# Kernel tuning notes

Measured on AMD Instinct MI355X. Metric: run time of the kernel, lower is better.

The kernel has to match this reference:

```python
import jax, jax.numpy as jnp
import numpy as np

N, C, H, W = 1024, 16, 32, 32
E = 4096


def setup_inputs() -> dict:
    key = jax.random.key(0)
    ks = jax.random.split(key, 10)
    feats = jax.random.normal(ks[0], (N, C, H, W), dtype=jnp.float32)
    src = jax.random.randint(ks[1], (E,), 0, N)
    dst = jax.random.randint(ks[2], (E,), 0, N)
    sign = jax.random.randint(ks[3], (E,), 0, 2) * 2 - 1  # values in {-1, +1}
    edges = jnp.stack([src, sign, dst], axis=1).astype(jnp.int64)
    s = 0.05
    w1 = jax.random.normal(ks[4], (2 * C, 3 * C, 3, 3), dtype=jnp.float32) * s
    b1 = jnp.zeros((2 * C,), dtype=jnp.float32)
    w2 = jax.random.normal(ks[5], (2 * C, 2 * C, 3, 3), dtype=jnp.float32) * s
    b2 = jnp.zeros((2 * C,), dtype=jnp.float32)
    w3 = jax.random.normal(ks[6], (C, 2 * C, 3, 3), dtype=jnp.float32) * s
    b3 = jnp.zeros((C,), dtype=jnp.float32)
    return {"feats": feats, "edges": edges, "w1": w1, "b1": b1,
            "w2": w2, "b2": b2, "w3": w3, "b3": b3}


def _pool_edges(edges, feats, positive):
    # Bidirectional gather + scatter_add over selected edges.
    # Mask-by-zero keeps shapes static (equivalent math to torch.where selection).
    sign = edges[:, 1]
    mask = (sign > 0) if positive else (sign < 0)
    w = mask.astype(feats.dtype)[:, None, None, None]
    src = edges[:, 0]
    dst = edges[:, 2]
    pooled = jnp.zeros_like(feats)
    pooled = pooled.at[dst].add(feats[src] * w)  # src -> dst
    pooled = pooled.at[src].add(feats[dst] * w)  # dst -> src
    return pooled


def _conv(x, w, b):
    y = jax.lax.conv_general_dilated(
        x, w, window_strides=(1, 1), padding=((1, 1), (1, 1)),
        dimension_numbers=("NCHW", "OIHW", "NCHW"))
    return y + b[None, :, None, None]


def _leaky(x):
    return jax.nn.leaky_relu(x, negative_slope=0.1)


def reference(feats, edges, w1, b1, w2, b2, w3, b3):
    pos = _pool_edges(edges, feats, positive=True)
    neg = _pool_edges(edges, feats, positive=False)
    x = jnp.concatenate([feats, pos, neg], axis=1)  # [N, 3C, H, W]
    x = _leaky(_conv(x, w1, b1))
    x = _leaky(_conv(x, w2, b2))
    x = _leaky(_conv(x, w3, b3))
    return x
```

## Files before the change

### kernel.cpp

```cpp
#include <hip/hip_runtime.h>


#define NIMG 1024
#define CHW  16384
#define NEDGE 4096
#define MAXD 64

#define ICP1 56
#define ICP2 40
#define XSZ (34*34*ICP1)
#define WSZ (14*32*32)

#define WG1N (14*32*32)
#define WG2N (9*32*32)
#define WG3N (9*16*32)
#define WGTOT (WG1N+WG2N+WG3N)

typedef __attribute__((ext_vector_type(8))) _Float16 half8;
typedef __attribute__((ext_vector_type(4))) _Float16 half4;
typedef __attribute__((ext_vector_type(4))) float float4v;

__device__ __forceinline__ float leaky(float x) { return x > 0.f ? x : 0.1f * x; }

__global__ __launch_bounds__(256) void prep_kernel(
    const float* __restrict__ feats, _Float16* __restrict__ fcl,
    const int* __restrict__ edges, int* __restrict__ deg, int* __restrict__ adj,
    const float* __restrict__ w1, const float* __restrict__ w2,
    const float* __restrict__ w3, _Float16* __restrict__ wg)
{
    const int b = blockIdx.x, tid = threadIdx.x;
    if (b < NIMG) {
        const int n = b;
        const float* fb = feats + (size_t)n * CHW;
        _Float16*    ob = fcl   + (size_t)n * 1024 * 16;
        const int p0 = tid * 4;
        float4v t[16];
        #pragma unroll
        for (int c = 0; c < 16; ++c) t[c] = *(const float4v*)(fb + (c << 10) + p0);
        #pragma unroll
        for (int u = 0; u < 4; ++u) {
            half8 v0, v1;
            #pragma unroll
            for (int c = 0; c < 8; ++c) { v0[c] = (_Float16)t[c][u]; v1[c] = (_Float16)t[c+8][u]; }
            *(half8*)(ob + (p0+u)*16)     = v0;
            *(half8*)(ob + (p0+u)*16 + 8) = v1;
        }
        return;
    }
    const int e = (b - NIMG) * 256 + tid;
    const bool is64 = (edges[1] == 0);
    int s, sg, d;
    if (is64) { s = edges[6*e]; sg = edges[6*e + 2]; d = edges[6*e + 4]; }
    else      { s = edges[3*e]; sg = edges[3*e + 1]; d = edges[3*e + 2]; }
    const int tag_d = (d << 1) | (int)(sg > 0);
    const int tag_s = (s << 1) | (int)(sg > 0);
    int i = atomicAdd(&deg[s], 1); if (i < MAXD) adj[(s << 6) + i] = tag_d;
    int j = atomicAdd(&deg[d], 1); if (j < MAXD) adj[(d << 6) + j] = tag_s;

    for (int t = e; t < WGTOT; t += NEDGE) {
        _Float16 val = (_Float16)0.f;
        if (t < WG1N) {
            int ks = t >> 10, oc = (t >> 5) & 31, j32 = t & 31;
            int k = ks*32 + j32;
            if (k < 432) { int tap = k / 48, ic = k - tap*48;
                           val = (_Float16)w1[(oc*48 + ic)*9 + tap]; }
        } else if (t < WG1N + WG2N) {
            int u = t - WG1N;
            int ks = u >> 10, oc = (u >> 5) & 31, j32 = u & 31;
            int k = ks*32 + j32;
            int tap = k >> 5, ic = k & 31;
            val = (_Float16)w2[(oc*32 + ic)*9 + tap];
        } else {
            int u = t - (WG1N + WG2N);
            int ks = u >> 9, oc = (u >> 5) & 15, j32 = u & 31;
            int k = ks*32 + j32;
            int tap = k >> 5, ic = k & 31;
            val = (_Float16)w3[(oc*32 + ic)*9 + tap];
        }
        wg[t] = val;
    }
}

__global__ __launch_bounds__(512, 2) void conv_kernel(
    const _Float16* __restrict__ fcl,
    const int* __restrict__ deg, const int* __restrict__ adj,
    const _Float16* __restrict__ wg,
    const float* __restrict__ b1, const float* __restrict__ b2,
    const float* __restrict__ b3, float* __restrict__ out)
{
    __shared__ __align__(16) _Float16 Xs[XSZ];
    __shared__ __align__(16) _Float16 Ws[WSZ];
    const int n    = blockIdx.x;
    const int tid  = threadIdx.x;
    const int wave = tid >> 6;
    const int lane = tid & 63;
    const int col  = lane & 15;
    const int quad = lane >> 4;

    {
        const half8* fc = (const half8*)(fcl + (size_t)n * CHW);
        int m = deg[n]; if (m > MAXD) m = MAXD;
        const int* al = adj + (n << 6);
        #pragma unroll 2
        for (int h = 0; h < 2; ++h) {
            const int p = tid + h*512;
            const int base = (((p >> 5) + 1)*34 + (p & 31) + 1) * ICP1;
            *(half8*)(Xs + base)     = fc[2*p];
            *(half8*)(Xs + base + 8) = fc[2*p + 1];
            float ap[16], an[16];
            #pragma unroll
            for (int c = 0; c < 16; ++c) { ap[c] = 0.f; an[c] = 0.f; }
            int i = 0;
            for (; i + 4 <= m; i += 4) {
                int v0 = al[i], v1 = al[i+1], v2 = al[i+2], v3 = al[i+3];
                const half8* f0 = (const half8*)(fcl + (size_t)(v0 >> 1) * CHW);
                const half8* f1 = (const half8*)(fcl + (size_t)(v1 >> 1) * CHW);
                const half8* f2 = (const half8*)(fcl + (size_t)(v2 >> 1) * CHW);
                const half8* f3 = (const half8*)(fcl + (size_t)(v3 >> 1) * CHW);
                half8 x00 = f0[2*p], x01 = f0[2*p+1];
                half8 x10 = f1[2*p], x11 = f1[2*p+1];
                half8 x20 = f2[2*p], x21 = f2[2*p+1];
                half8 x30 = f3[2*p], x31 = f3[2*p+1];
                if (v0 & 1) { for (int c = 0; c < 8; ++c) { ap[c] += (float)x00[c]; ap[c+8] += (float)x01[c]; } }
                else        { for (int c = 0; c < 8; ++c) { an[c] += (float)x00[c]; an[c+8] += (float)x01[c]; } }
                if (v1 & 1) { for (int c = 0; c < 8; ++c) { ap[c] += (float)x10[c]; ap[c+8] += (float)x11[c]; } }
                else        { for (int c = 0; c < 8; ++c) { an[c] += (float)x10[c]; an[c+8] += (float)x11[c]; } }
                if (v2 & 1) { for (int c = 0; c < 8; ++c) { ap[c] += (float)x20[c]; ap[c+8] += (float)x21[c]; } }
                else        { for (int c = 0; c < 8; ++c) { an[c] += (float)x20[c]; an[c+8] += (float)x21[c]; } }
                if (v3 & 1) { for (int c = 0; c < 8; ++c) { ap[c] += (float)x30[c]; ap[c+8] += (float)x31[c]; } }
                else        { for (int c = 0; c < 8; ++c) { an[c] += (float)x30[c]; an[c+8] += (float)x31[c]; } }
            }
            for (; i < m; ++i) {
                const int v = al[i];
                const half8* fb = (const half8*)(fcl + (size_t)(v >> 1) * CHW);
                half8 x0 = fb[2*p], x1 = fb[2*p + 1];
                if (v & 1) {
                    #pragma unroll
                    for (int c = 0; c < 8; ++c) { ap[c] += (float)x0[c]; ap[c+8] += (float)x1[c]; }
                } else {
                    #pragma unroll
                    for (int c = 0; c < 8; ++c) { an[c] += (float)x0[c]; an[c+8] += (float)x1[c]; }
                }
            }
            half8 h0, h1, h2, h3;
            #pragma unroll
            for (int c = 0; c < 8; ++c) { h0[c] = (_Float16)ap[c]; h1[c] = (_Float16)ap[c+8];
                                          h2[c] = (_Float16)an[c]; h3[c] = (_Float16)an[c+8]; }
            *(half8*)(Xs + base + 16) = h0;
            *(half8*)(Xs + base + 24) = h1;
            *(half8*)(Xs + base + 32) = h2;
            *(half8*)(Xs + base + 40) = h3;
        }
        {
            const half8* src = (const half8*)wg;
            half8* dst = (half8*)Ws;
            for (int t = tid; t < WG1N/8; t += 512) dst[t] = src[t];
        }
        if (tid < 132) {
            int hp, wp;
            if      (tid < 34)  { hp = 0;        wp = tid; }
            else if (tid < 68)  { hp = 33;       wp = tid - 34; }
            else if (tid < 100) { hp = tid - 67; wp = 0; }
            else                { hp = tid - 99; wp = 33; }
            int hb = (hp*34 + wp) * ICP1;
            #pragma unroll
            for (int t = 0; t < 6; ++t) *(half8*)(Xs + hb + t*8) = (half8)0;
        }
    }
    __syncthreads();

    float4v acc[2][8];

    {
        #pragma unroll
        for (int m = 0; m < 2; ++m)
            #pragma unroll
            for (int j = 0; j < 8; ++j) acc[m][j] = (float4v){0.f,0.f,0.f,0.f};
        int pixb[8];
        #pragma unroll
        for (int j = 0; j < 8; ++j) {
            int p = wave*128 + j*16 + col;
            pixb[j] = ((p >> 5)*34 + (p & 31)) * ICP1;
        }
        const int abase = col*32 + quad*8;
        #pragma unroll
        for (int ks = 0; ks < 14; ++ks) {
            int kq  = ks*32 + quad*8;
            int tap = kq / 48;
            int off = 0;
            if (tap < 9) {
                int ic0 = kq - tap*48;
                int dh = tap / 3, dw = tap - dh*3;
                off = (dh*34 + dw)*ICP1 + ic0;
            }
            half8 a0 = *(const half8*)(Ws + ks*1024 + abase);
            half8 a1 = *(const half8*)(Ws + ks*1024 + 512 + abase);
            #pragma unroll
            for (int j = 0; j < 8; ++j) {
                half8 b = *(const half8*)(Xs + pixb[j] + off);
                acc[0][j] = __builtin_amdgcn_mfma_f32_16x16x32_f16(a0, b, acc[0][j], 0, 0, 0);
                acc[1][j] = __builtin_amdgcn_mfma_f32_16x16x32_f16(a1, b, acc[1][j], 0, 0, 0);
            }
        }
    }
    __syncthreads();

    {
        if (tid < 132) {
            int hp, wp;
            if      (tid < 34)  { hp = 0;        wp = tid; }
            else if (tid < 68)  { hp = 33;       wp = tid - 34; }
            else if (tid < 100) { hp = tid - 67; wp = 0; }
            else                { hp = tid - 99; wp = 33; }
            int hb = (hp*34 + wp) * ICP2;
            #pragma unroll
            for (int t = 0; t < 4; ++t) *(half8*)(Xs + hb + t*8) = (half8)0;
        }
        float bv[2][4];
        #pragma unroll
        for (int m = 0; m < 2; ++m)
            #pragma unroll
            for (int r = 0; r < 4; ++r) bv[m][r] = b1[m*16 + quad*4 + r];
        #pragma unroll
        for (int m = 0; m < 2; ++m)
            #pragma unroll
            for (int j = 0; j < 8; ++j) {
                int p = wave*128 + j*16 + col;
                _Float16* y = Xs + ((((p>>5)+1)*34) + (p&31) + 1)*ICP2 + m*16 + quad*4;
                half4 v;
                #pragma unroll
                for (int r = 0; r < 4; ++r) v[r] = (_Float16)leaky(acc[m][j][r] + bv[m][r]);
                *(half4*)y = v;
            }
        {
            const half8* src = (const half8*)(wg + WG1N);
            half8* dst = (half8*)Ws;
            for (int t = tid; t < WG2N/8; t += 512) dst[t] = src[t];
        }
    }
    __syncthreads();

    {
        #pragma unroll
        for (int m = 0; m < 2; ++m)
            #pragma unroll
            for (int j = 0; j < 8; ++j) acc[m][j] = (float4v){0.f,0.f,0.f,0.f};
        int pixb[8];
        #pragma unroll
        for (int j = 0; j < 8; ++j) {
            int p = wave*128 + j*16 + col;
            pixb[j] = ((p >> 5)*34 + (p & 31)) * ICP2;
        }
        const int abase = col*32 + quad*8;
        #pragma unroll
        for (int ks = 0; ks < 9; ++ks) {
            int kq  = ks*32 + quad*8;
            int tap = kq >> 5, ic0 = kq & 31;
            int dh = tap / 3, dw = tap - dh*3;
            int off = (dh*34 + dw)*ICP2 + ic0;
            half8 a0 = *(const half8*)(Ws + ks*1024 + abase);
            half8 a1 = *(const half8*)(Ws + ks*1024 + 512 + abase);
            #pragma unroll
            for (int j = 0; j < 8; ++j) {
                half8 b = *(const half8*)(Xs + pixb[j] + off);
                acc[0][j] = __builtin_amdgcn_mfma_f32_16x16x32_f16(a0, b, acc[0][j], 0, 0, 0);
                acc[1][j] = __builtin_amdgcn_mfma_f32_16x16x32_f16(a1, b, acc[1][j], 0, 0, 0);
            }
        }
    }
    __syncthreads();

    {
        float bv[2][4];
        #pragma unroll
        for (int m = 0; m < 2; ++m)
            #pragma unroll
            for (int r = 0; r < 4; ++r) bv[m][r] = b2[m*16 + quad*4 + r];
        #pragma unroll
        for (int m = 0; m < 2; ++m)
            #pragma unroll
            for (int j = 0; j < 8; ++j) {
                int p = wave*128 + j*16 + col;
                _Float16* y = Xs + ((((p>>5)+1)*34) + (p&31) + 1)*ICP2 + m*16 + quad*4;
                half4 v;
                #pragma unroll
                for (int r = 0; r < 4; ++r) v[r] = (_Float16)leaky(acc[m][j][r] + bv[m][r]);
                *(half4*)y = v;
            }
        {
            const half8* src = (const half8*)(wg + WG1N + WG2N);
            half8* dst = (half8*)Ws;
            for (int t = tid; t < WG3N/8; t += 512) dst[t] = src[t];
        }
    }
    __syncthreads();

    {
        float4v a3[8];
        #pragma unroll
        for (int j = 0; j < 8; ++j) a3[j] = (float4v){0.f,0.f,0.f,0.f};
        int pixb[8];
        #pragma unroll
        for (int j = 0; j < 8; ++j) {
            int p = wave*128 + j*16 + col;
            pixb[j] = ((p >> 5)*34 + (p & 31)) * ICP2;
        }
        const int abase = col*32 + quad*8;
        #pragma unroll
        for (int ks = 0; ks < 9; ++ks) {
            int kq  = ks*32 + quad*8;
            int tap = kq >> 5, ic0 = kq & 31;
            int dh = tap / 3, dw = tap - dh*3;
            int off = (dh*34 + dw)*ICP2 + ic0;
            half8 a0 = *(const half8*)(Ws + ks*512 + abase);
            #pragma unroll
            for (int j = 0; j < 8; ++j) {
                half8 b = *(const half8*)(Xs + pixb[j] + off);
                a3[j] = __builtin_amdgcn_mfma_f32_16x16x32_f16(a0, b, a3[j], 0, 0, 0);
            }
        }
        float bv[4];
        #pragma unroll
        for (int r = 0; r < 4; ++r) bv[r] = b3[quad*4 + r];
        float* op = out + (size_t)n * CHW;
        #pragma unroll
        for (int j = 0; j < 8; ++j) {
            int p = wave*128 + j*16 + col;
            #pragma unroll
            for (int r = 0; r < 4; ++r)
                op[(quad*4 + r)*1024 + p] = leaky(a3[j][r] + bv[r]);
        }
    }
}

extern "C" void kernel_launch(void* const* d_in, const int* in_sizes, int n_in,
                              void* d_out, int out_size, void* d_ws, size_t ws_size,
                              hipStream_t stream) {
    const float* feats = (const float*)d_in[0];
    const int*   edges = (const int*)  d_in[1];
    const float* w1 = (const float*)d_in[2];
    const float* b1 = (const float*)d_in[3];
    const float* w2 = (const float*)d_in[4];
    const float* b2 = (const float*)d_in[5];
    const float* w3 = (const float*)d_in[6];
    const float* b3 = (const float*)d_in[7];
    float* out = (float*)d_out;

    _Float16* fcl = (_Float16*)d_ws;
    int* deg = (int*)((char*)d_ws + (32u << 20));
    int* adj = deg + NIMG;
    _Float16* wg = (_Float16*)((char*)d_ws + (32u << 20) + 4096 + NIMG*MAXD*4);

    hipMemsetAsync(deg, 0, NIMG * sizeof(int), stream);
    prep_kernel<<<dim3(NIMG + NEDGE/256), dim3(256), 0, stream>>>(
        feats, fcl, edges, deg, adj, w1, w2, w3, wg);
    conv_kernel<<<dim3(NIMG), dim3(512), 0, stream>>>(fcl, deg, adj, wg,
                                                      b1, b2, b3, out);
}
```

Before: 227.2 us.

## Split each image into two half-height blocks with halo recompute, read weights from global

The conv kernel now launches two blocks per image. Each block handles 16 output rows and recomputes a 3-row halo for the first two conv layers, so the three fused convolutions need no inter-block communication. The weight staging buffer in LDS is removed: MFMA A-operands are loaded straight from global memory, and the smaller activation tile raises the occupancy target to 4 blocks per CU. The costs are redundant halo work in both the gather and the convs, extra neighbour-gather traffic, and per-k-step global weight loads that depend on cache hits.

```diff
diff --git a/kernel.cpp b/kernel.cpp
--- a/kernel.cpp
+++ b/kernel.cpp
@@ -8,8 +8,8 @@
 
 #define ICP1 56
 #define ICP2 40
-#define XSZ (34*34*ICP1)
-#define WSZ (14*32*32)
+#define XROWS 20
+#define XSZ (XROWS*34*ICP1)
 
 #define WG1N (14*32*32)
 #define WG2N (9*32*32)
@@ -81,7 +81,61 @@
     }
 }
 
-__global__ __launch_bounds__(512, 2) void conv_kernel(
+__device__ __forceinline__ void stage_gather(
+    const half8* __restrict__ fc, const _Float16* __restrict__ fcl,
+    const int* __restrict__ al, int m, int q, int woff, int bh,
+    _Float16* __restrict__ Xs)
+{
+    const int p = bh*416 + q;
+    const int base = (((q >> 5) + woff)*34 + (q & 31) + 1) * ICP1;
+    *(half8*)(Xs + base)     = fc[2*p];
+    *(half8*)(Xs + base + 8) = fc[2*p + 1];
+    float ap[16], an[16];
+    #pragma unroll
+    for (int c = 0; c < 16; ++c) { ap[c] = 0.f; an[c] = 0.f; }
+    int i = 0;
+    for (; i + 4 <= m; i += 4) {
+        int v0 = al[i], v1 = al[i+1], v2 = al[i+2], v3 = al[i+3];
+        const half8* f0 = (const half8*)(fcl + (size_t)(v0 >> 1) * CHW);
+        const half8* f1 = (const half8*)(fcl + (size_t)(v1 >> 1) * CHW);
+        const half8* f2 = (const half8*)(fcl + (size_t)(v2 >> 1) * CHW);
+        const half8* f3 = (const half8*)(fcl + (size_t)(v3 >> 1) * CHW);
+        half8 x00 = f0[2*p], x01 = f0[2*p+1];
+        half8 x10 = f1[2*p], x11 = f1[2*p+1];
+        half8 x20 = f2[2*p], x21 = f2[2*p+1];
+        half8 x30 = f3[2*p], x31 = f3[2*p+1];
+        if (v0 & 1) { for (int c = 0; c < 8; ++c) { ap[c] += (float)x00[c]; ap[c+8] += (float)x01[c]; } }
+        else        { for (int c = 0; c < 8; ++c) { an[c] += (float)x00[c]; an[c+8] += (float)x01[c]; } }
+        if (v1 & 1) { for (int c = 0; c < 8; ++c) { ap[c] += (float)x10[c]; ap[c+8] += (float)x11[c]; } }
+        else        { for (int c = 0; c < 8; ++c) { an[c] += (float)x10[c]; an[c+8] += (float)x11[c]; } }
+        if (v2 & 1) { for (int c = 0; c < 8; ++c) { ap[c] += (float)x20[c]; ap[c+8] += (float)x21[c]; } }
+        else        { for (int c = 0; c < 8; ++c) { an[c] += (float)x20[c]; an[c+8] += (float)x21[c]; } }
+        if (v3 & 1) { for (int c = 0; c < 8; ++c) { ap[c] += (float)x30[c]; ap[c+8] += (float)x31[c]; } }
+        else        { for (int c = 0; c < 8; ++c) { an[c] += (float)x30[c]; an[c+8] += (float)x31[c]; } }
+    }
+    for (; i < m; ++i) {
+        const int v = al[i];
+        const half8* fb = (const half8*)(fcl + (size_t)(v >> 1) * CHW);
+        half8 x0 = fb[2*p], x1 = fb[2*p + 1];
+        if (v & 1) {
+            #pragma unroll
+            for (int c = 0; c < 8; ++c) { ap[c] += (float)x0[c]; ap[c+8] += (float)x1[c]; }
+        } else {
+            #pragma unroll
+            for (int c = 0; c < 8; ++c) { an[c] += (float)x0[c]; an[c+8] += (float)x1[c]; }
+        }
+    }
+    half8 h0, h1, h2, h3;
+    #pragma unroll
+    for (int c = 0; c < 8; ++c) { h0[c] = (_Float16)ap[c]; h1[c] = (_Float16)ap[c+8];
+                                  h2[c] = (_Float16)an[c]; h3[c] = (_Float16)an[c+8]; }
+    *(half8*)(Xs + base + 16) = h0;
+    *(half8*)(Xs + base + 24) = h1;
+    *(half8*)(Xs + base + 32) = h2;
+    *(half8*)(Xs + base + 40) = h3;
+}
+
+__global__ __launch_bounds__(512, 4) void conv_kernel(
     const _Float16* __restrict__ fcl,
     const int* __restrict__ deg, const int* __restrict__ adj,
     const _Float16* __restrict__ wg,
@@ -89,98 +143,50 @@
     const float* __restrict__ b3, float* __restrict__ out)
 {
     __shared__ __align__(16) _Float16 Xs[XSZ];
-    __shared__ __align__(16) _Float16 Ws[WSZ];
-    const int n    = blockIdx.x;
+    const int bid  = blockIdx.x;
+    const int n    = bid >> 1;
+    const int bh   = bid & 1;
     const int tid  = threadIdx.x;
     const int wave = tid >> 6;
     const int lane = tid & 63;
     const int col  = lane & 15;
     const int quad = lane >> 4;
+    const int woff = bh ? 0 : 1;
+
+    const _Float16* wg1 = wg;
+    const _Float16* wg2 = wg + WG1N;
+    const _Float16* wg3 = wg + WG1N + WG2N;
 
     {
         const half8* fc = (const half8*)(fcl + (size_t)n * CHW);
         int m = deg[n]; if (m > MAXD) m = MAXD;
         const int* al = adj + (n << 6);
-        #pragma unroll 2
-        for (int h = 0; h < 2; ++h) {
-            const int p = tid + h*512;
-            const int base = (((p >> 5) + 1)*34 + (p & 31) + 1) * ICP1;
-            *(half8*)(Xs + base)     = fc[2*p];
-            *(half8*)(Xs + base + 8) = fc[2*p + 1];
-            float ap[16], an[16];
-            #pragma unroll
-            for (int c = 0; c < 16; ++c) { ap[c] = 0.f; an[c] = 0.f; }
-            int i = 0;
-            for (; i + 4 <= m; i += 4) {
-                int v0 = al[i], v1 = al[i+1], v2 = al[i+2], v3 = al[i+3];
-                const half8* f0 = (const half8*)(fcl + (size_t)(v0 >> 1) * CHW);
-                const half8* f1 = (const half8*)(fcl + (size_t)(v1 >> 1) * CHW);
-                const half8* f2 = (const half8*)(fcl + (size_t)(v2 >> 1) * CHW);
-                const half8* f3 = (const half8*)(fcl + (size_t)(v3 >> 1) * CHW);
-                half8 x00 = f0[2*p], x01 = f0[2*p+1];
-                half8 x10 = f1[2*p], x11 = f1[2*p+1];
-                half8 x20 = f2[2*p], x21 = f2[2*p+1];
-                half8 x30 = f3[2*p], x31 = f3[2*p+1];
-                if (v0 & 1) { for (int c = 0; c < 8; ++c) { ap[c] += (float)x00[c]; ap[c+8] += (float)x01[c]; } }
-                else        { for (int c = 0; c < 8; ++c) { an[c] += (float)x00[c]; an[c+8] += (float)x01[c]; } }
-                if (v1 & 1) { for (int c = 0; c < 8; ++c) { ap[c] += (float)x10[c]; ap[c+8] += (float)x11[c]; } }
-                else        { for (int c = 0; c < 8; ++c) { an[c] += (float)x10[c]; an[c+8] += (float)x11[c]; } }
-                if (v2 & 1) { for (int c = 0; c < 8; ++c) { ap[c] += (float)x20[c]; ap[c+8] += (float)x21[c]; } }
-                else        { for (int c = 0; c < 8; ++c) { an[c] += (float)x20[c]; an[c+8] += (float)x21[c]; } }
-                if (v3 & 1) { for (int c = 0; c < 8; ++c) { ap[c] += (float)x30[c]; ap[c+8] += (float)x31[c]; } }
-                else        { for (int c = 0; c < 8; ++c) { an[c] += (float)x30[c]; an[c+8] += (float)x31[c]; } }
-            }
-            for (; i < m; ++i) {
-                const int v = al[i];
-                const half8* fb = (const half8*)(fcl + (size_t)(v >> 1) * CHW);
-                half8 x0 = fb[2*p], x1 = fb[2*p + 1];
-                if (v & 1) {
-                    #pragma unroll
-                    for (int c = 0; c < 8; ++c) { ap[c] += (float)x0[c]; ap[c+8] += (float)x1[c]; }
-                } else {
-                    #pragma unroll
-                    for (int c = 0; c < 8; ++c) { an[c] += (float)x0[c]; an[c+8] += (float)x1[c]; }
-                }
-            }
-            half8 h0, h1, h2, h3;
-            #pragma unroll
-            for (int c = 0; c < 8; ++c) { h0[c] = (_Float16)ap[c]; h1[c] = (_Float16)ap[c+8];
-                                          h2[c] = (_Float16)an[c]; h3[c] = (_Float16)an[c+8]; }
-            *(half8*)(Xs + base + 16) = h0;
-            *(half8*)(Xs + base + 24) = h1;
-            *(half8*)(Xs + base + 32) = h2;
-            *(half8*)(Xs + base + 40) = h3;
-        }
-        {
-            const half8* src = (const half8*)wg;
-            half8* dst = (half8*)Ws;
-            for (int t = tid; t < WG1N/8; t += 512) dst[t] = src[t];
-        }
-        if (tid < 132) {
-            int hp, wp;
-            if      (tid < 34)  { hp = 0;        wp = tid; }
-            else if (tid < 68)  { hp = 33;       wp = tid - 34; }
-            else if (tid < 100) { hp = tid - 67; wp = 0; }
-            else                { hp = tid - 99; wp = 33; }
-            int hb = (hp*34 + wp) * ICP1;
+        stage_gather(fc, fcl, al, m, tid, woff, bh, Xs);
+        if (tid < 96)
+            stage_gather(fc, fcl, al, m, 512 + tid, woff, bh, Xs);
+        if (tid >= 440) {
+            int z = tid - 440, row, cx;
+            if (z < 34) { row = bh ? 19 : 0; cx = z; }
+            else { int t2 = z - 34; row = (t2 >> 1) + woff; cx = (t2 & 1) ? 33 : 0; }
+            int hb = (row*34 + cx) * ICP1;
             #pragma unroll
             for (int t = 0; t < 6; ++t) *(half8*)(Xs + hb + t*8) = (half8)0;
         }
     }
     __syncthreads();
 
-    float4v acc[2][8];
-
-    {
-        #pragma unroll
-        for (int m = 0; m < 2; ++m)
-            #pragma unroll
-            for (int j = 0; j < 8; ++j) acc[m][j] = (float4v){0.f,0.f,0.f,0.f};
-        int pixb[8];
-        #pragma unroll
-        for (int j = 0; j < 8; ++j) {
-            int p = wave*128 + j*16 + col;
-            pixb[j] = ((p >> 5)*34 + (p & 31)) * ICP1;
+    float4v acc[2][5];
+
+    {
+        #pragma unroll
+        for (int m = 0; m < 2; ++m)
+            #pragma unroll
+            for (int j = 0; j < 5; ++j) acc[m][j] = (float4v){0.f,0.f,0.f,0.f};
+        int pixb[5];
+        #pragma unroll
+        for (int j = 0; j < 5; ++j) {
+            int q = (wave + j*8)*16 + col;
+            pixb[j] = ((q >> 5)*34 + (q & 31)) * ICP1;
         }
         const int abase = col*32 + quad*8;
         #pragma unroll
@@ -193,26 +199,26 @@
                 int dh = tap / 3, dw = tap - dh*3;
                 off = (dh*34 + dw)*ICP1 + ic0;
             }
-            half8 a0 = *(const half8*)(Ws + ks*1024 + abase);
-            half8 a1 = *(const half8*)(Ws + ks*1024 + 512 + abase);
-            #pragma unroll
-            for (int j = 0; j < 8; ++j) {
-                half8 b = *(const half8*)(Xs + pixb[j] + off);
-                acc[0][j] = __builtin_amdgcn_mfma_f32_16x16x32_f16(a0, b, acc[0][j], 0, 0, 0);
-                acc[1][j] = __builtin_amdgcn_mfma_f32_16x16x32_f16(a1, b, acc[1][j], 0, 0, 0);
-            }
-        }
-    }
-    __syncthreads();
-
-    {
-        if (tid < 132) {
-            int hp, wp;
-            if      (tid < 34)  { hp = 0;        wp = tid; }
-            else if (tid < 68)  { hp = 33;       wp = tid - 34; }
-            else if (tid < 100) { hp = tid - 67; wp = 0; }
-            else                { hp = tid - 99; wp = 33; }
-            int hb = (hp*34 + wp) * ICP2;
+            half8 a0 = *(const half8*)(wg1 + ks*1024 + abase);
+            half8 a1 = *(const half8*)(wg1 + ks*1024 + 512 + abase);
+            #pragma unroll
+            for (int j = 0; j < 5; ++j) {
+                if (wave + j*8 < 36) {
+                    half8 b = *(const half8*)(Xs + pixb[j] + off);
+                    acc[0][j] = __builtin_amdgcn_mfma_f32_16x16x32_f16(a0, b, acc[0][j], 0, 0, 0);
+                    acc[1][j] = __builtin_amdgcn_mfma_f32_16x16x32_f16(a1, b, acc[1][j], 0, 0, 0);
+                }
+            }
+        }
+    }
+    __syncthreads();
+
+    {
+        if (tid < 70) {
+            int row, cx;
+            if (tid < 34) { row = bh ? 18 : 0; cx = tid; }
+            else { int t2 = tid - 34; row = (t2 >> 1) + woff; cx = (t2 & 1) ? 33 : 0; }
+            int hb = (row*34 + cx) * ICP2;
             #pragma unroll
             for (int t = 0; t < 4; ++t) *(half8*)(Xs + hb + t*8) = (half8)0;
         }
@@ -224,32 +230,29 @@
         #pragma unroll
         for (int m = 0; m < 2; ++m)
             #pragma unroll
-            for (int j = 0; j < 8; ++j) {
-                int p = wave*128 + j*16 + col;
-                _Float16* y = Xs + ((((p>>5)+1)*34) + (p&31) + 1)*ICP2 + m*16 + quad*4;
-                half4 v;
-                #pragma unroll
-                for (int r = 0; r < 4; ++r) v[r] = (_Float16)leaky(acc[m][j][r] + bv[m][r]);
-                *(half4*)y = v;
-            }
-        {
-            const half8* src = (const half8*)(wg + WG1N);
-            half8* dst = (half8*)Ws;
-            for (int t = tid; t < WG2N/8; t += 512) dst[t] = src[t];
-        }
-    }
-    __syncthreads();
-
-    {
-        #pragma unroll
-        for (int m = 0; m < 2; ++m)
-            #pragma unroll
-            for (int j = 0; j < 8; ++j) acc[m][j] = (float4v){0.f,0.f,0.f,0.f};
-        int pixb[8];
-        #pragma unroll
-        for (int j = 0; j < 8; ++j) {
-            int p = wave*128 + j*16 + col;
-            pixb[j] = ((p >> 5)*34 + (p & 31)) * ICP2;
+            for (int j = 0; j < 5; ++j) {
+                if (wave + j*8 < 36) {
+                    int q = (wave + j*8)*16 + col;
+                    _Float16* y = Xs + (((q>>5) + woff)*34 + (q&31) + 1)*ICP2 + m*16 + quad*4;
+                    half4 v;
+                    #pragma unroll
+                    for (int r = 0; r < 4; ++r) v[r] = (_Float16)leaky(acc[m][j][r] + bv[m][r]);
+                    *(half4*)y = v;
+                }
+            }
+    }
+    __syncthreads();
+
+    {
+        #pragma unroll
+        for (int m = 0; m < 2; ++m)
+            #pragma unroll
+            for (int j = 0; j < 5; ++j) acc[m][j] = (float4v){0.f,0.f,0.f,0.f};
+        int pixb[5];
+        #pragma unroll
+        for (int j = 0; j < 5; ++j) {
+            int q = (wave + j*8)*16 + col;
+            pixb[j] = ((q >> 5)*34 + (q & 31)) * ICP2;
         }
         const int abase = col*32 + quad*8;
         #pragma unroll
@@ -258,19 +261,29 @@
             int tap = kq >> 5, ic0 = kq & 31;
             int dh = tap / 3, dw = tap - dh*3;
             int off = (dh*34 + dw)*ICP2 + ic0;
-            half8 a0 = *(const half8*)(Ws + ks*1024 + abase);
-            half8 a1 = *(const half8*)(Ws + ks*1024 + 512 + abase);
-            #pragma unroll
-            for (int j = 0; j < 8; ++j) {
-                half8 b = *(const half8*)(Xs + pixb[j] + off);
-                acc[0][j] = __builtin_amdgcn_mfma_f32_16x16x32_f16(a0, b, acc[0][j], 0, 0, 0);
-                acc[1][j] = __builtin_amdgcn_mfma_f32_16x16x32_f16(a1, b, acc[1][j], 0, 0, 0);
-            }
-        }
-    }
-    __syncthreads();
-
-    {
+            half8 a0 = *(const half8*)(wg2 + ks*1024 + abase);
+            half8 a1 = *(const half8*)(wg2 + ks*1024 + 512 + abase);
+            #pragma unroll
+            for (int j = 0; j < 5; ++j) {
+                if (wave + j*8 < 34) {
+                    half8 b = *(const half8*)(Xs + pixb[j] + off);
+                    acc[0][j] = __builtin_amdgcn_mfma_f32_16x16x32_f16(a0, b, acc[0][j], 0, 0, 0);
+                    acc[1][j] = __builtin_amdgcn_mfma_f32_16x16x32_f16(a1, b, acc[1][j], 0, 0, 0);
+                }
+            }
+        }
+    }
+    __syncthreads();
+
+    {
+        if (tid < 68) {
+            int row, cx;
+            if (tid < 34) { row = bh ? 17 : 0; cx = tid; }
+            else { int t2 = tid - 34; row = (t2 >> 1) + woff; cx = (t2 & 1) ? 33 : 0; }
+            int hb = (row*34 + cx) * ICP2;
+            #pragma unroll
+            for (int t = 0; t < 4; ++t) *(half8*)(Xs + hb + t*8) = (half8)0;
+        }
         float bv[2][4];
         #pragma unroll
         for (int m = 0; m < 2; ++m)
@@ -279,31 +292,28 @@
         #pragma unroll
         for (int m = 0; m < 2; ++m)
             #pragma unroll
-            for (int j = 0; j < 8; ++j) {
-                int p = wave*128 + j*16 + col;
-                _Float16* y = Xs + ((((p>>5)+1)*34) + (p&31) + 1)*ICP2 + m*16 + quad*4;
-                half4 v;
-                #pragma unroll
-                for (int r = 0; r < 4; ++r) v[r] = (_Float16)leaky(acc[m][j][r] + bv[m][r]);
-                *(half4*)y = v;
-            }
-        {
-            const half8* src = (const half8*)(wg + WG1N + WG2N);
-            half8* dst = (half8*)Ws;
-            for (int t = tid; t < WG3N/8; t += 512) dst[t] = src[t];
-        }
-    }
-    __syncthreads();
-
-    {
-        float4v a3[8];
-        #pragma unroll
-        for (int j = 0; j < 8; ++j) a3[j] = (float4v){0.f,0.f,0.f,0.f};
-        int pixb[8];
-        #pragma unroll
-        for (int j = 0; j < 8; ++j) {
-            int p = wave*128 + j*16 + col;
-            pixb[j] = ((p >> 5)*34 + (p & 31)) * ICP2;
+            for (int j = 0; j < 5; ++j) {
+                if (wave + j*8 < 34) {
+                    int q = (wave + j*8)*16 + col;
+                    _Float16* y = Xs + (((q>>5) + woff)*34 + (q&31) + 1)*ICP2 + m*16 + quad*4;
+                    half4 v;
+                    #pragma unroll
+                    for (int r = 0; r < 4; ++r) v[r] = (_Float16)leaky(acc[m][j][r] + bv[m][r]);
+                    *(half4*)y = v;
+                }
+            }
+    }
+    __syncthreads();
+
+    {
+        float4v a3[4];
+        #pragma unroll
+        for (int j = 0; j < 4; ++j) a3[j] = (float4v){0.f,0.f,0.f,0.f};
+        int pixb[4];
+        #pragma unroll
+        for (int j = 0; j < 4; ++j) {
+            int q = (wave + j*8)*16 + col;
+            pixb[j] = ((q >> 5)*34 + (q & 31)) * ICP2;
         }
         const int abase = col*32 + quad*8;
         #pragma unroll
@@ -312,9 +322,9 @@
             int tap = kq >> 5, ic0 = kq & 31;
             int dh = tap / 3, dw = tap - dh*3;
             int off = (dh*34 + dw)*ICP2 + ic0;
-            half8 a0 = *(const half8*)(Ws + ks*512 + abase);
-            #pragma unroll
-            for (int j = 0; j < 8; ++j) {
+            half8 a0 = *(const half8*)(wg3 + ks*512 + abase);
+            #pragma unroll
+            for (int j = 0; j < 4; ++j) {
                 half8 b = *(const half8*)(Xs + pixb[j] + off);
                 a3[j] = __builtin_amdgcn_mfma_f32_16x16x32_f16(a0, b, a3[j], 0, 0, 0);
             }
@@ -324,8 +334,9 @@
         for (int r = 0; r < 4; ++r) bv[r] = b3[quad*4 + r];
         float* op = out + (size_t)n * CHW;
         #pragma unroll
-        for (int j = 0; j < 8; ++j) {
-            int p = wave*128 + j*16 + col;
+        for (int j = 0; j < 4; ++j) {
+            int q = (wave + j*8)*16 + col;
+            int p = bh*512 + q;
             #pragma unroll
             for (int r = 0; r < 4; ++r)
                 op[(quad*4 + r)*1024 + p] = leaky(a3[j][r] + bv[r]);
@@ -354,6 +365,6 @@
     hipMemsetAsync(deg, 0, NIMG * sizeof(int), stream);
     prep_kernel<<<dim3(NIMG + NEDGE/256), dim3(256), 0, stream>>>(
         feats, fcl, edges, deg, adj, w1, w2, w3, wg);
-    conv_kernel<<<dim3(NIMG), dim3(512), 0, stream>>>(fcl, deg, adj, wg,
-                                                      b1, b2, b3, out);
+    conv_kernel<<<dim3(2*NIMG), dim3(512), 0, stream>>>(fcl, deg, adj, wg,
+                                                        b1, b2, b3, out);
 }
```

After: 232.5 us. 2.3% more time.

## Double block size to 1024 threads and prefetch weights into registers before barriers

Applied to the files above, without the earlier changes.

The conv kernel now launches 1024 threads per image instead of 512, so each wave handles 64 pixels with half the MFMA accumulators and each thread gathers one pixel. Weight tiles for the next conv stage are loaded from global into registers before the epilogue and written to LDS afterwards, overlapping global latency with compute. The first batch of neighbour gathers is issued alongside the self-feature and weight loads. Launch bounds (1024,4) may force register spilling, and with about 75 KB of LDS per block occupancy is likely limited to two blocks per CU.

```diff
diff --git a/kernel.cpp b/kernel.cpp
--- a/kernel.cpp
+++ b/kernel.cpp
@@ -81,7 +81,40 @@
     }
 }
 
-__global__ __launch_bounds__(512, 2) void conv_kernel(
+__device__ __forceinline__ void gaccum(
+    const _Float16* __restrict__ fcl, const int* __restrict__ al,
+    int i, int m, int p, float* __restrict__ ap, float* __restrict__ an)
+{
+    for (; i + 4 <= m; i += 4) {
+        int v[4]; half8 x[8];
+        #pragma unroll
+        for (int u = 0; u < 4; ++u) v[u] = al[i+u];
+        #pragma unroll
+        for (int u = 0; u < 4; ++u) {
+            const half8* f = (const half8*)(fcl + (size_t)(v[u] >> 1) * CHW);
+            x[2*u] = f[2*p]; x[2*u+1] = f[2*p+1];
+        }
+        #pragma unroll
+        for (int u = 0; u < 4; ++u) {
+            if (v[u] & 1) { for (int c = 0; c < 8; ++c) { ap[c] += (float)x[2*u][c]; ap[c+8] += (float)x[2*u+1][c]; } }
+            else          { for (int c = 0; c < 8; ++c) { an[c] += (float)x[2*u][c]; an[c+8] += (float)x[2*u+1][c]; } }
+        }
+    }
+    for (; i < m; ++i) {
+        const int v = al[i];
+        const half8* fb = (const half8*)(fcl + (size_t)(v >> 1) * CHW);
+        half8 x0 = fb[2*p], x1 = fb[2*p + 1];
+        if (v & 1) {
+            #pragma unroll
+            for (int c = 0; c < 8; ++c) { ap[c] += (float)x0[c]; ap[c+8] += (float)x1[c]; }
+        } else {
+            #pragma unroll
+            for (int c = 0; c < 8; ++c) { an[c] += (float)x0[c]; an[c+8] += (float)x1[c]; }
+        }
+    }
+}
+
+__global__ __launch_bounds__(1024, 4) void conv_kernel(
     const _Float16* __restrict__ fcl,
     const int* __restrict__ deg, const int* __restrict__ adj,
     const _Float16* __restrict__ wg,
@@ -101,61 +134,29 @@
         const half8* fc = (const half8*)(fcl + (size_t)n * CHW);
         int m = deg[n]; if (m > MAXD) m = MAXD;
         const int* al = adj + (n << 6);
-        #pragma unroll 2
-        for (int h = 0; h < 2; ++h) {
-            const int p = tid + h*512;
-            const int base = (((p >> 5) + 1)*34 + (p & 31) + 1) * ICP1;
-            *(half8*)(Xs + base)     = fc[2*p];
-            *(half8*)(Xs + base + 8) = fc[2*p + 1];
-            float ap[16], an[16];
-            #pragma unroll
-            for (int c = 0; c < 16; ++c) { ap[c] = 0.f; an[c] = 0.f; }
-            int i = 0;
-            for (; i + 4 <= m; i += 4) {
-                int v0 = al[i], v1 = al[i+1], v2 = al[i+2], v3 = al[i+3];
-                const half8* f0 = (const half8*)(fcl + (size_t)(v0 >> 1) * CHW);
-                const half8* f1 = (const half8*)(fcl + (size_t)(v1 >> 1) * CHW);
-                const half8* f2 = (const half8*)(fcl + (size_t)(v2 >> 1) * CHW);
-                const half8* f3 = (const half8*)(fcl + (size_t)(v3 >> 1) * CHW);
-                half8 x00 = f0[2*p], x01 = f0[2*p+1];
-                half8 x10 = f1[2*p], x11 = f1[2*p+1];
-                half8 x20 = f2[2*p], x21 = f2[2*p+1];
-                half8 x30 = f3[2*p], x31 = f3[2*p+1];
-                if (v0 & 1) { for (int c = 0; c < 8; ++c) { ap[c] += (float)x00[c]; ap[c+8] += (float)x01[c]; } }
-                else        { for (int c = 0; c < 8; ++c) { an[c] += (float)x00[c]; an[c+8] += (float)x01[c]; } }
-                if (v1 & 1) { for (int c = 0; c < 8; ++c) { ap[c] += (float)x10[c]; ap[c+8] += (float)x11[c]; } }
-                else        { for (int c = 0; c < 8; ++c) { an[c] += (float)x10[c]; an[c+8] += (float)x11[c]; } }
-                if (v2 & 1) { for (int c = 0; c < 8; ++c) { ap[c] += (float)x20[c]; ap[c+8] += (float)x21[c]; } }
-                else        { for (int c = 0; c < 8; ++c) { an[c] += (float)x20[c]; an[c+8] += (float)x21[c]; } }
-                if (v3 & 1) { for (int c = 0; c < 8; ++c) { ap[c] += (float)x30[c]; ap[c+8] += (float)x31[c]; } }
-                else        { for (int c = 0; c < 8; ++c) { an[c] += (float)x30[c]; an[c+8] += (float)x31[c]; } }
-            }
-            for (; i < m; ++i) {
-                const int v = al[i];
-                const half8* fb = (const half8*)(fcl + (size_t)(v >> 1) * CHW);
-                half8 x0 = fb[2*p], x1 = fb[2*p + 1];
-                if (v & 1) {
-                    #pragma unroll
-                    for (int c = 0; c < 8; ++c) { ap[c] += (float)x0[c]; ap[c+8] += (float)x1[c]; }
-                } else {
-                    #pragma unroll
-                    for (int c = 0; c < 8; ++c) { an[c] += (float)x0[c]; an[c+8] += (float)x1[c]; }
-                }
-            }
-            half8 h0, h1, h2, h3;
-            #pragma unroll
-            for (int c = 0; c < 8; ++c) { h0[c] = (_Float16)ap[c]; h1[c] = (_Float16)ap[c+8];
-                                          h2[c] = (_Float16)an[c]; h3[c] = (_Float16)an[c+8]; }
-            *(half8*)(Xs + base + 16) = h0;
-            *(half8*)(Xs + base + 24) = h1;
-            *(half8*)(Xs + base + 32) = h2;
-            *(half8*)(Xs + base + 40) = h3;
-        }
-        {
-            const half8* src = (const half8*)wg;
-            half8* dst = (half8*)Ws;
-            for (int t = tid; t < WG1N/8; t += 512) dst[t] = src[t];
-        }
+        const int p = tid;
+        const int base = (((p >> 5) + 1)*34 + (p & 31) + 1) * ICP1;
+
+        const half8* wsrc = (const half8*)wg;
+        half8 wa = wsrc[tid];
+        half8 wb; if (tid < 768) wb = wsrc[tid + 1024];
+        half8 s0 = fc[2*p], s1 = fc[2*p + 1];
+
+        const int nb = m < 4 ? m : 4;
+        int v0[4]; half8 x0[8];
+        #pragma unroll
+        for (int u = 0; u < 4; ++u)
+            if (u < nb) {
+                v0[u] = al[u];
+                const half8* f = (const half8*)(fcl + (size_t)(v0[u] >> 1) * CHW);
+                x0[2*u] = f[2*p]; x0[2*u+1] = f[2*p + 1];
+            }
+
+        half8* wdst = (half8*)Ws;
+        wdst[tid] = wa;
+        if (tid < 768) wdst[tid + 1024] = wb;
+        *(half8*)(Xs + base)     = s0;
+        *(half8*)(Xs + base + 8) = s1;
         if (tid < 132) {
             int hp, wp;
             if      (tid < 34)  { hp = 0;        wp = tid; }
@@ -166,20 +167,39 @@
             #pragma unroll
             for (int t = 0; t < 6; ++t) *(half8*)(Xs + hb + t*8) = (half8)0;
         }
-    }
-    __syncthreads();
-
-    float4v acc[2][8];
-
-    {
-        #pragma unroll
-        for (int m = 0; m < 2; ++m)
-            #pragma unroll
-            for (int j = 0; j < 8; ++j) acc[m][j] = (float4v){0.f,0.f,0.f,0.f};
-        int pixb[8];
-        #pragma unroll
-        for (int j = 0; j < 8; ++j) {
-            int p = wave*128 + j*16 + col;
+
+        float ap[16], an[16];
+        #pragma unroll
+        for (int c = 0; c < 16; ++c) { ap[c] = 0.f; an[c] = 0.f; }
+        #pragma unroll
+        for (int u = 0; u < 4; ++u)
+            if (u < nb) {
+                if (v0[u] & 1) { for (int c = 0; c < 8; ++c) { ap[c] += (float)x0[2*u][c]; ap[c+8] += (float)x0[2*u+1][c]; } }
+                else           { for (int c = 0; c < 8; ++c) { an[c] += (float)x0[2*u][c]; an[c+8] += (float)x0[2*u+1][c]; } }
+            }
+        gaccum(fcl, al, nb, m, p, ap, an);
+        half8 h0, h1, h2, h3;
+        #pragma unroll
+        for (int c = 0; c < 8; ++c) { h0[c] = (_Float16)ap[c]; h1[c] = (_Float16)ap[c+8];
+                                      h2[c] = (_Float16)an[c]; h3[c] = (_Float16)an[c+8]; }
+        *(half8*)(Xs + base + 16) = h0;
+        *(half8*)(Xs + base + 24) = h1;
+        *(half8*)(Xs + base + 32) = h2;
+        *(half8*)(Xs + base + 40) = h3;
+    }
+    __syncthreads();
+
+    float4v acc[2][4];
+
+    {
+        #pragma unroll
+        for (int m = 0; m < 2; ++m)
+            #pragma unroll
+            for (int j = 0; j < 4; ++j) acc[m][j] = (float4v){0.f,0.f,0.f,0.f};
+        int pixb[4];
+        #pragma unroll
+        for (int j = 0; j < 4; ++j) {
+            int p = wave*64 + j*16 + col;
             pixb[j] = ((p >> 5)*34 + (p & 31)) * ICP1;
         }
         const int abase = col*32 + quad*8;
@@ -196,7 +216,7 @@
             half8 a0 = *(const half8*)(Ws + ks*1024 + abase);
             half8 a1 = *(const half8*)(Ws + ks*1024 + 512 + abase);
             #pragma unroll
-            for (int j = 0; j < 8; ++j) {
+            for (int j = 0; j < 4; ++j) {
                 half8 b = *(const half8*)(Xs + pixb[j] + off);
                 acc[0][j] = __builtin_amdgcn_mfma_f32_16x16x32_f16(a0, b, acc[0][j], 0, 0, 0);
                 acc[1][j] = __builtin_amdgcn_mfma_f32_16x16x32_f16(a1, b, acc[1][j], 0, 0, 0);
@@ -206,6 +226,10 @@
     __syncthreads();
 
     {
+        const half8* wsrc = (const half8*)(wg + WG1N);
+        half8 wa = wsrc[tid];
+        half8 wb; if (tid < 128) wb = wsrc[tid + 1024];
+
         if (tid < 132) {
             int hp, wp;
             if      (tid < 34)  { hp = 0;        wp = tid; }
@@ -224,31 +248,29 @@
         #pragma unroll
         for (int m = 0; m < 2; ++m)
             #pragma unroll
-            for (int j = 0; j < 8; ++j) {
-                int p = wave*128 + j*16 + col;
+            for (int j = 0; j < 4; ++j) {
+                int p = wave*64 + j*16 + col;
                 _Float16* y = Xs + ((((p>>5)+1)*34) + (p&31) + 1)*ICP2 + m*16 + quad*4;
                 half4 v;
                 #pragma unroll
                 for (int r = 0; r < 4; ++r) v[r] = (_Float16)leaky(acc[m][j][r] + bv[m][r]);
                 *(half4*)y = v;
             }
-        {
-            const half8* src = (const half8*)(wg + WG1N);
-            half8* dst = (half8*)Ws;
-            for (int t = tid; t < WG2N/8; t += 512) dst[t] = src[t];
-        }
-    }
-    __syncthreads();
-
-    {
-        #pragma unroll
-        for (int m = 0; m < 2; ++m)
-            #pragma unroll
-            for (int j = 0; j < 8; ++j) acc[m][j] = (float4v){0.f,0.f,0.f,0.f};
-        int pixb[8];
-        #pragma unroll
-        for (int j = 0; j < 8; ++j) {
-            int p = wave*128 + j*16 + col;
+        half8* wdst = (half8*)Ws;
+        wdst[tid] = wa;
+        if (tid < 128) wdst[tid + 1024] = wb;
+    }
+    __syncthreads();
+
+    {
+        #pragma unroll
+        for (int m = 0; m < 2; ++m)
+            #pragma unroll
+            for (int j = 0; j < 4; ++j) acc[m][j] = (float4v){0.f,0.f,0.f,0.f};
+        int pixb[4];
+        #pragma unroll
+        for (int j = 0; j < 4; ++j) {
+            int p = wave*64 + j*16 + col;
             pixb[j] = ((p >> 5)*34 + (p & 31)) * ICP2;
         }
         const int abase = col*32 + quad*8;
@@ -261,7 +283,7 @@
             half8 a0 = *(const half8*)(Ws + ks*1024 + abase);
             half8 a1 = *(const half8*)(Ws + ks*1024 + 512 + abase);
             #pragma unroll
-            for (int j = 0; j < 8; ++j) {
+            for (int j = 0; j < 4; ++j) {
                 half8 b = *(const half8*)(Xs + pixb[j] + off);
                 acc[0][j] = __builtin_amdgcn_mfma_f32_16x16x32_f16(a0, b, acc[0][j], 0, 0, 0);
                 acc[1][j] = __builtin_amdgcn_mfma_f32_16x16x32_f16(a1, b, acc[1][j], 0, 0, 0);
@@ -271,6 +293,9 @@
     __syncthreads();
 
     {
+        const half8* wsrc = (const half8*)(wg + WG1N + WG2N);
+        half8 wa; if (tid < 576) wa = wsrc[tid];
+
         float bv[2][4];
         #pragma unroll
         for (int m = 0; m < 2; ++m)
@@ -279,30 +304,26 @@
         #pragma unroll
         for (int m = 0; m < 2; ++m)
             #pragma unroll
-            for (int j = 0; j < 8; ++j) {
-                int p = wave*128 + j*16 + col;
+            for (int j = 0; j < 4; ++j) {
+                int p = wave*64 + j*16 + col;
                 _Float16* y = Xs + ((((p>>5)+1)*34) + (p&31) + 1)*ICP2 + m*16 + quad*4;
                 half4 v;
                 #pragma unroll
                 for (int r = 0; r < 4; ++r) v[r] = (_Float16)leaky(acc[m][j][r] + bv[m][r]);
                 *(half4*)y = v;
             }
-        {
-            const half8* src = (const half8*)(wg + WG1N + WG2N);
-            half8* dst = (half8*)Ws;
-            for (int t = tid; t < WG3N/8; t += 512) dst[t] = src[t];
-        }
-    }
-    __syncthreads();
-
-    {
-        float4v a3[8];
-        #pragma unroll
-        for (int j = 0; j < 8; ++j) a3[j] = (float4v){0.f,0.f,0.f,0.f};
-        int pixb[8];
-        #pragma unroll
-        for (int j = 0; j < 8; ++j) {
-            int p = wave*128 + j*16 + col;
+        if (tid < 576) ((half8*)Ws)[tid] = wa;
+    }
+    __syncthreads();
+
+    {
+        float4v a3[4];
+        #pragma unroll
+        for (int j = 0; j < 4; ++j) a3[j] = (float4v){0.f,0.f,0.f,0.f};
+        int pixb[4];
+        #pragma unroll
+        for (int j = 0; j < 4; ++j) {
+            int p = wave*64 + j*16 + col;
             pixb[j] = ((p >> 5)*34 + (p & 31)) * ICP2;
         }
         const int abase = col*32 + quad*8;
@@ -314,7 +335,7 @@
             int off = (dh*34 + dw)*ICP2 + ic0;
             half8 a0 = *(const half8*)(Ws + ks*512 + abase);
             #pragma unroll
-            for (int j = 0; j < 8; ++j) {
+            for (int j = 0; j < 4; ++j) {
                 half8 b = *(const half8*)(Xs + pixb[j] + off);
                 a3[j] = __builtin_amdgcn_mfma_f32_16x16x32_f16(a0, b, a3[j], 0, 0, 0);
             }
@@ -324,8 +345,8 @@
         for (int r = 0; r < 4; ++r) bv[r] = b3[quad*4 + r];
         float* op = out + (size_t)n * CHW;
         #pragma unroll
-        for (int j = 0; j < 8; ++j) {
-            int p = wave*128 + j*16 + col;
+        for (int j = 0; j < 4; ++j) {
+            int p = wave*64 + j*16 + col;
             #pragma unroll
             for (int r = 0; r < 4; ++r)
                 op[(quad*4 + r)*1024 + p] = leaky(a3[j][r] + bv[r]);
@@ -354,6 +375,6 @@
     hipMemsetAsync(deg, 0, NIMG * sizeof(int), stream);
     prep_kernel<<<dim3(NIMG + NEDGE/256), dim3(256), 0, stream>>>(
         feats, fcl, edges, deg, adj, w1, w2, w3, wg);
-    conv_kernel<<<dim3(NIMG), dim3(512), 0, stream>>>(fcl, deg, adj, wg,
-                                                      b1, b2, b3, out);
+    conv_kernel<<<dim3(NIMG), dim3(1024), 0, stream>>>(fcl, deg, adj, wg,
+                                                       b1, b2, b3, out);
 }
```

After: 226.7 us. About the same (-0.2%).
